# Optimization experiments

Hardware: AMD Instinct MI355X
Metric: run time of the kernel (lower is better)

The kernel has to match this reference:

```python
import jax, jax.numpy as jnp
import numpy as np

D_MODEL, D_STATE, D_CONV, EXPAND = 1024, 16, 4, 2
D_INNER = EXPAND * D_MODEL
BATCH, SEQ = 2, 2048


def setup_inputs() -> dict:
    key = jax.random.key(0)
    ks = jax.random.split(key, 10)
    inv = lambda n: 1.0 / np.sqrt(n)
    return {
        "x": jax.random.normal(ks[0], (BATCH, SEQ, D_MODEL), jnp.float32),
        "in_proj_w": jax.random.uniform(ks[1], (2 * D_INNER, D_MODEL), jnp.float32, -inv(D_MODEL), inv(D_MODEL)),
        "conv_w": jax.random.uniform(ks[2], (D_INNER, D_INNER, D_CONV), jnp.float32, -inv(D_INNER * D_CONV), inv(D_INNER * D_CONV)),
        "conv_b": jax.random.uniform(ks[3], (D_INNER,), jnp.float32, -inv(D_INNER * D_CONV), inv(D_INNER * D_CONV)),
        "dt_w": jax.random.uniform(ks[4], (D_INNER, D_INNER), jnp.float32, -inv(D_INNER), inv(D_INNER)),
        "dt_b": jax.random.uniform(ks[5], (D_INNER,), jnp.float32, -inv(D_INNER), inv(D_INNER)),
        "A_log": jax.random.normal(ks[6], (D_INNER, D_STATE), jnp.float32) * 0.01,
        "D": jnp.ones((D_INNER,), jnp.float32),
        "B_w": jax.random.uniform(ks[7], (D_STATE, D_INNER), jnp.float32, -inv(D_INNER), inv(D_INNER)),
        "C_w": jax.random.uniform(ks[8], (D_STATE, D_INNER), jnp.float32, -inv(D_INNER), inv(D_INNER)),
        "out_w": jax.random.uniform(ks[9], (D_MODEL, D_INNER), jnp.float32, -inv(D_INNER), inv(D_INNER)),
    }


def _forward(x, in_proj_w, conv_w, conv_b, dt_w, dt_b, A_log, D, B_w, C_w, out_w):
    xz = x @ in_proj_w.T                      # [b, l, 2*d_inner]
    xc, z = jnp.split(xz, 2, axis=-1)
    # causal depthful conv1d (full channel mixing, left-padded)
    h = jnp.transpose(xc, (0, 2, 1))          # [b, d, l]
    h = jnp.pad(h, ((0, 0), (0, 0), (D_CONV - 1, 0)))
    h = jax.lax.conv_general_dilated(h, conv_w, (1,), 'VALID',
                                     dimension_numbers=('NCH', 'OIH', 'NCH'))
    h = h + conv_b[None, :, None]
    u = jnp.transpose(h, (0, 2, 1))           # [b, l, d_inner]

    dt = jnp.clip(jax.nn.sigmoid(u @ dt_w.T + dt_b), 1e-4, 1.0)  # [b, l, d]
    A = -jnp.exp(A_log)                       # [d, n]
    Bm = u @ B_w.T                            # [b, l, n]
    Cm = u @ C_w.T                            # [b, l, n]

    # time-major scan over the recurrence
    u_t = jnp.transpose(u, (1, 0, 2))
    dt_t = jnp.transpose(dt, (1, 0, 2))
    B_t = jnp.transpose(Bm, (1, 0, 2))
    C_t = jnp.transpose(Cm, (1, 0, 2))

    def step(state, inp):
        ut, dtt, bt, ct = inp                 # [b,d], [b,d], [b,n], [b,n]
        dA = jnp.exp(jnp.clip(dtt[:, :, None] * A, -5.0, 5.0))   # [b,d,n]
        dB = dtt[:, :, None] * bt[:, None, :] * ut[:, :, None]   # [b,d,n]
        state = dA * state + dB + 1e-6
        y = jnp.sum(state * ct[:, None, :], axis=-1) + D * ut    # [b,d]
        return state, y

    state0 = jnp.zeros((x.shape[0], D_INNER, D_STATE), x.dtype)
    _, ys = jax.lax.scan(step, state0, (u_t, dt_t, B_t, C_t))
    y = jnp.transpose(ys, (1, 0, 2))          # [b, l, d_inner]
    y = y * jax.nn.silu(z)
    return y @ out_w.T                        # [b, l, d_model]


def reference(x, in_proj_w, conv_w, conv_b, dt_w, dt_b, A_log, D, B_w, C_w, out_w):
    return _forward(x, in_proj_w, conv_w, conv_b, dt_w, dt_b, A_log, D, B_w, C_w, out_w)
```

## Files before the change

### kernel.cpp

```cpp
#include <hip/hip_runtime.h>

#define BATCHN 2
#define SEQL   2048
#define DM     1024
#define DI     2048
#define DSN    16
#define MTOT   (BATCHN * SEQL)
#define PADL   (SEQL + 3)
#define NC     64
#define CL     (SEQL / NC)
#define BCKS   8

typedef __attribute__((ext_vector_type(8))) __bf16 bf16x8;
typedef __attribute__((ext_vector_type(4))) float f32x4;

__device__ __forceinline__ unsigned short f2b(float f) {
    union { float f; unsigned u; } v; v.f = f;
    unsigned r = v.u + 0x7FFF + ((v.u >> 16) & 1);
    return (unsigned short)(r >> 16);
}
__device__ __forceinline__ float b2f(unsigned short b) {
    union { float f; unsigned u; } v; v.u = ((unsigned)b) << 16;
    return v.f;
}

__device__ __forceinline__ void gl_lds16(const void* g, void* l) {
    __builtin_amdgcn_global_load_lds(
        (const __attribute__((address_space(1))) unsigned int*)g,
        (__attribute__((address_space(3))) unsigned int*)l, 16, 0, 0);
}

__device__ __forceinline__ void swz(int& bx, int& by) {
    int gx = gridDim.x, gy = gridDim.y;
    int lin = blockIdx.y * gx + blockIdx.x;
    int xcd = lin & 7, k = lin >> 3;
    int rw = gx >> 1, rh = gy >> 2;
    by = (xcd >> 1) * rh + k / rw;
    bx = (xcd & 1) * rw + k % rw;
}

#define NB_XCVT (MTOT * DM / 4 / 256)
__global__ void cvt_x_all(const float* __restrict__ src, unsigned short* __restrict__ dst) {
    int blk = blockIdx.x;
    if (blk < NB_XCVT) {
        int i = blk * 256 + threadIdx.x;
        int b = i >> 19;
        float4 v = ((const float4*)src)[i];
        ushort4 o;
        o.x = f2b(v.x); o.y = f2b(v.y); o.z = f2b(v.z); o.w = f2b(v.w);
        ((ushort4*)dst)[i + (b + 1) * (3 * DM / 4)] = o;
    } else {
        int i = (blk - NB_XCVT) * 256 + threadIdx.x;
        if (i < BATCHN * 3 * DM) {
            int b = i / (3 * DM);
            int r = i % (3 * DM);
            dst[(size_t)b * PADL * DM + r] = 0;
        }
    }
}

#define NB_CONVW (DI * DI / 256)
#define NB_TP    ((DM / 32) * (DI / 32))
#define NB_IPZ   (DI * DM / 4 / 256)
#define NB_DTW   (DI * DI / 4 / 256)
#define NB_OW    (DM * DI / 4 / 256)
#define NB_BW    (DSN * DI / 4 / 256 + 1)
__global__ void __launch_bounds__(256)
cvt_w_all(const float* __restrict__ convw, const float* __restrict__ ipw,
          const float* __restrict__ dtw, const float* __restrict__ ow,
          const float* __restrict__ bw, const float* __restrict__ cw,
          unsigned short* __restrict__ wk, unsigned short* __restrict__ Pt,
          unsigned short* __restrict__ ipz, unsigned short* __restrict__ dtwb,
          unsigned short* __restrict__ owb, unsigned short* __restrict__ bcb)
{
    __shared__ float tile[32][33];
    int blk = blockIdx.x;
    int t = threadIdx.x;
    if (blk < NB_CONVW) {
        int i = blk * 256 + t;
        float4 v = ((const float4*)convw)[i];
        wk[0 * (size_t)DI * DI + i] = f2b(v.x);
        wk[1 * (size_t)DI * DI + i] = f2b(v.y);
        wk[2 * (size_t)DI * DI + i] = f2b(v.z);
        wk[3 * (size_t)DI * DI + i] = f2b(v.w);
        return;
    }
    blk -= NB_CONVW;
    if (blk < NB_TP) {
        int ct = (blk & 31) * 32, it = (blk >> 5) * 32;
        int tx = t & 31, ty = t >> 5;
#pragma unroll
        for (int r = 0; r < 4; ++r)
            tile[ty + r * 8][tx] = ipw[(size_t)(it + ty + r * 8) * DM + ct + tx];
        __syncthreads();
#pragma unroll
        for (int r = 0; r < 4; ++r)
            Pt[(size_t)(ct + ty + r * 8) * DI + it + tx] = f2b(tile[tx][ty + r * 8]);
        return;
    }
    blk -= NB_TP;
    const float* src;
    unsigned short* dst;
    int n4;
    if (blk < NB_IPZ) {
        src = ipw + (size_t)DI * DM; dst = ipz; n4 = DI * DM / 4;
    } else if ((blk -= NB_IPZ) < NB_DTW) {
        src = dtw; dst = dtwb; n4 = DI * DI / 4;
    } else if ((blk -= NB_DTW) < NB_OW) {
        src = ow; dst = owb; n4 = DM * DI / 4;
    } else if ((blk -= NB_OW) < NB_BW) {
        src = bw; dst = bcb; n4 = DSN * DI / 4;
    } else {
        blk -= NB_BW;
        src = cw; dst = bcb + (size_t)DSN * DI; n4 = DSN * DI / 4;
    }
    int i = blk * 256 + t;
    if (i < n4) {
        float4 v = ((const float4*)src)[i];
        ushort4 o;
        o.x = f2b(v.x); o.y = f2b(v.y); o.z = f2b(v.z); o.w = f2b(v.w);
        ((ushort4*)dst)[i] = o;
    }
}

template<int MODE>
__global__ void __launch_bounds__(256)
gemm_bt(const unsigned short* __restrict__ Abase,
        const unsigned short* __restrict__ Bbase,
        const float* __restrict__ bias,
        unsigned short* __restrict__ out_bf,
        float* __restrict__ out_f,
        int K)
{
    __shared__ __align__(16) unsigned short As[128 * 64];
    __shared__ __align__(16) unsigned short Bs[128 * 64];

    const int t = threadIdx.x;
    const int lane = t & 63;
    const int wave = t >> 6;
    const int wm = wave & 1, wn = wave >> 1;
    int bx, by;
    swz(bx, by);
    const int m0 = by * 128, n0 = bx * 128;
    const int srow = t >> 3;
    const int scol = (t & 7) * 8;
    const int gcol = (((t & 7) ^ (srow & 7))) * 8;

    f32x4 acc[4][4];
#pragma unroll
    for (int i = 0; i < 4; ++i)
#pragma unroll
        for (int j = 0; j < 4; ++j)
            acc[i][j] = f32x4{0.f, 0.f, 0.f, 0.f};

    const unsigned short* arow[4];
    const unsigned short* brow[4];
#pragma unroll
    for (int i = 0; i < 4; ++i) {
        int rg = m0 + srow + i * 32;
        arow[i] = Abase + (size_t)rg * K;
        int ng = n0 + srow + i * 32;
        brow[i] = Bbase + (size_t)ng * K;
    }
    for (int k0 = 0; k0 < K; k0 += 64) {
#pragma unroll
        for (int i = 0; i < 4; ++i)
            gl_lds16(arow[i] + k0 + gcol, &As[(size_t)(srow + i * 32) * 64 + scol]);
#pragma unroll
        for (int i = 0; i < 4; ++i)
            gl_lds16(brow[i] + k0 + gcol, &Bs[(size_t)(srow + i * 32) * 64 + scol]);
        __syncthreads();
        const int qa = (lane >> 4) * 8;
        const int am = lane & 15;
        const int sw = (am & 7) << 3;
#pragma unroll
        for (int kk = 0; kk < 64; kk += 32) {
            bf16x8 af[4], bfv[4];
#pragma unroll
            for (int i = 0; i < 4; ++i)
                af[i] = *(const bf16x8*)&As[(wm * 64 + i * 16 + am) * 64 + ((kk + qa) ^ sw)];
#pragma unroll
            for (int j = 0; j < 4; ++j)
                bfv[j] = *(const bf16x8*)&Bs[(wn * 64 + j * 16 + am) * 64 + ((kk + qa) ^ sw)];
#pragma unroll
            for (int i = 0; i < 4; ++i)
#pragma unroll
                for (int j = 0; j < 4; ++j)
                    acc[i][j] = __builtin_amdgcn_mfma_f32_16x16x32_bf16(
                        af[i], bfv[j], acc[i][j], 0, 0, 0);
        }
        __syncthreads();
    }

    const int erow0 = m0 + wm * 64;
    const int ecol0 = n0 + wn * 64 + (lane & 15);
    const int rq = (lane >> 4) * 4;
#pragma unroll
    for (int i = 0; i < 4; ++i) {
#pragma unroll
        for (int j = 0; j < 4; ++j) {
            int col = ecol0 + j * 16;
#pragma unroll
            for (int r = 0; r < 4; ++r) {
                int row = erow0 + i * 16 + rq + r;
                float v = acc[i][j][r];
                if (MODE == 3) {
                    out_f[(size_t)row * DM + col] = v;
                } else {
                    out_bf[(size_t)row * DI + col] = f2b(v);
                }
            }
        }
    }
}


#define ABUF8(b) ((b) * 16384)
#define BBUF8(b) (32768 + (b) * 8192)

#define STA8(buf, Mh, kt) do { const int kc_ = ((kt) & NTM) << 6; \
    gl_lds16(pAst + (size_t)((Mh) * 32) * SA + kc_, &lds[ABUF8(buf) + (Mh) * 8192 + ldsw]); \
    gl_lds16(pAst + (size_t)((Mh) * 32 + 128) * SA + kc_, &lds[ABUF8(buf) + (Mh) * 8192 + 4096 + ldsw]); \
} while (0)
#define STB8(buf, Nh, kt) do { const int kc_ = ((kt) & NTM) << 6; \
    gl_lds16(pBst + (size_t)((Nh) * 32) * SB + kc_, &lds[BBUF8(buf) + (Nh) * 4096 + ldsw]); \
} while (0)

#define LA8(buf, Mh) \
    a00 = *(const bf16x8*)&lds[ABUF8(buf) + (Mh) * 8192 + ar + c0]; \
    a01 = *(const bf16x8*)&lds[ABUF8(buf) + (Mh) * 8192 + ar + c1]; \
    a10 = *(const bf16x8*)&lds[ABUF8(buf) + (Mh) * 8192 + ar + 1024 + c0]; \
    a11 = *(const bf16x8*)&lds[ABUF8(buf) + (Mh) * 8192 + ar + 1024 + c1];
#define LB8(buf, Nh) \
    b00 = *(const bf16x8*)&lds[BBUF8(buf) + (Nh) * 4096 + br + c0]; \
    b01 = *(const bf16x8*)&lds[BBUF8(buf) + (Nh) * 4096 + br + c1]; \
    b10 = *(const bf16x8*)&lds[BBUF8(buf) + (Nh) * 4096 + br + 1024 + c0]; \
    b11 = *(const bf16x8*)&lds[BBUF8(buf) + (Nh) * 4096 + br + 1024 + c1];

#define MM8(Mh, Nh) \
    acc[(Mh)*2][(Nh)*2]     = __builtin_amdgcn_mfma_f32_16x16x32_bf16(a00, b00, acc[(Mh)*2][(Nh)*2], 0, 0, 0); \
    acc[(Mh)*2][(Nh)*2+1]   = __builtin_amdgcn_mfma_f32_16x16x32_bf16(a00, b10, acc[(Mh)*2][(Nh)*2+1], 0, 0, 0); \
    acc[(Mh)*2+1][(Nh)*2]   = __builtin_amdgcn_mfma_f32_16x16x32_bf16(a10, b00, acc[(Mh)*2+1][(Nh)*2], 0, 0, 0); \
    acc[(Mh)*2+1][(Nh)*2+1] = __builtin_amdgcn_mfma_f32_16x16x32_bf16(a10, b10, acc[(Mh)*2+1][(Nh)*2+1], 0, 0, 0); \
    acc[(Mh)*2][(Nh)*2]     = __builtin_amdgcn_mfma_f32_16x16x32_bf16(a01, b01, acc[(Mh)*2][(Nh)*2], 0, 0, 0); \
    acc[(Mh)*2][(Nh)*2+1]   = __builtin_amdgcn_mfma_f32_16x16x32_bf16(a01, b11, acc[(Mh)*2][(Nh)*2+1], 0, 0, 0); \
    acc[(Mh)*2+1][(Nh)*2]   = __builtin_amdgcn_mfma_f32_16x16x32_bf16(a11, b01, acc[(Mh)*2+1][(Nh)*2], 0, 0, 0); \
    acc[(Mh)*2+1][(Nh)*2+1] = __builtin_amdgcn_mfma_f32_16x16x32_bf16(a11, b11, acc[(Mh)*2+1][(Nh)*2+1], 0, 0, 0);

#define PH_MID \
    __builtin_amdgcn_s_barrier(); \
    asm volatile("s_waitcnt lgkmcnt(0)" ::: "memory"); \
    __builtin_amdgcn_sched_barrier(0); \
    __builtin_amdgcn_s_setprio(1);
#define PH_END \
    __builtin_amdgcn_s_setprio(0); \
    __builtin_amdgcn_s_barrier(); \
    __builtin_amdgcn_sched_barrier(0);
#define PH_END_W \
    __builtin_amdgcn_s_setprio(0); \
    asm volatile("s_waitcnt vmcnt(3)" ::: "memory"); \
    __builtin_amdgcn_s_barrier(); \
    __builtin_amdgcn_sched_barrier(0);

template<int MODE>
__global__ void __launch_bounds__(512, 1)
gemm8(const unsigned short* __restrict__ Abase,
      const unsigned short* __restrict__ Bbase,
      const float* __restrict__ bias,
      unsigned short* __restrict__ out_bf,
      float* __restrict__ out_f)
{
    constexpr int K   = (MODE == 0) ? 1024 : (MODE == 1) ? 4096 : 2048;
    constexpr int SA  = (MODE == 2 || MODE == 4) ? 2048 : 1024;
    constexpr int SB  = (MODE == 0) ? 1024 : (MODE == 1) ? 4096 : 2048;
    constexpr int NT  = K / 64;
    constexpr int NTM = NT - 1;
    constexpr int NI  = NT / 2;
    (void)out_f;

    __shared__ __align__(16) unsigned short lds[49152];

    const int t = threadIdx.x;
    const int lane = t & 63;
    const int wave = t >> 6;
    const int wm = wave >> 1;
    const int wn = wave & 1;
    int bx, by;
    swz(bx, by);
    const int m0 = by * 256, n0 = bx * 128;

    const unsigned short* Ap;
    if (MODE == 0)      Ap = Abase + ((size_t)(m0 >> 11) * PADL + 3 + (m0 & 2047)) * DM;
    else if (MODE == 1) Ap = Abase + ((size_t)(m0 >> 11) * PADL + (m0 & 2047)) * DM;
    else if (MODE == 4) Ap = Abase + (size_t)blockIdx.z * DI * DI + (size_t)m0 * SA;
    else                Ap = Abase + (size_t)m0 * SA;
    const unsigned short* Bp = Bbase + (size_t)n0 * SB;

    const int tr = t >> 3;
    const int rowg = ((tr >> 5) << 6) + (tr & 31);
    const int gcolb = ((t & 7) ^ (tr & 7)) << 3;
    const unsigned short* pAst = Ap + (size_t)rowg * SA + gcolb;
    const unsigned short* pBst = Bp + (size_t)rowg * SB + gcolb;
    const int ldsw = t * 8;

    const int am = lane & 15;
    const int qa = (lane >> 4) << 3;
    const int sw = (am & 7) << 3;
    const int c0 = qa ^ sw;
    const int c1 = (32 + qa) ^ sw;
    const int ar = wm * 2048 + am * 64;
    const int br = wn * 2048 + am * 64;

    f32x4 acc[4][4];
#pragma unroll
    for (int i = 0; i < 4; ++i)
#pragma unroll
        for (int j = 0; j < 4; ++j)
            acc[i][j] = f32x4{0.f, 0.f, 0.f, 0.f};

    bf16x8 a00, a01, a10, a11, b00, b01, b10, b11;

    STA8(0, 0, 0); STB8(0, 1, 0); STA8(0, 1, 0); STB8(0, 0, 0);
    STA8(1, 0, 1); STB8(1, 1, 1);
    asm volatile("s_waitcnt vmcnt(3)" ::: "memory");
    __builtin_amdgcn_s_barrier();
    __builtin_amdgcn_sched_barrier(0);

#pragma unroll 1
    for (int it = 0; it < NI; ++it) {
        const int ko  = 2 * it + 1;
        const int ke  = (2 * it + 2) & NTM;
        const int ko2 = (2 * it + 3) & NTM;
        LA8(0, 0) LB8(0, 0) STA8(1, 1, ko);
        PH_MID MM8(0, 0) PH_END
        LB8(0, 1) STB8(1, 0, ko);
        PH_MID MM8(0, 1) PH_END
        LA8(0, 1) STA8(0, 0, ke);
        PH_MID MM8(1, 1) PH_END
        LB8(0, 0) STB8(0, 1, ke);
        PH_MID MM8(1, 0) PH_END_W
        LA8(1, 0) LB8(1, 0) STA8(0, 1, ke);
        PH_MID MM8(0, 0) PH_END
        LB8(1, 1) STB8(0, 0, ke);
        PH_MID MM8(0, 1) PH_END
        LA8(1, 1) STA8(1, 0, ko2);
        PH_MID MM8(1, 1) PH_END
        LB8(1, 0) STB8(1, 1, ko2);
        PH_MID MM8(1, 0) PH_END_W
    }

    asm volatile("s_waitcnt vmcnt(0)" ::: "memory");

    const int rq = (lane >> 4) << 2;
    const int er = m0 + wm * 64;
    const int ec = n0 + wn * 64 + am;
#pragma unroll
    for (int mi = 0; mi < 4; ++mi) {
#pragma unroll
        for (int nj = 0; nj < 4; ++nj) {
            int col = ec + nj * 16;
#pragma unroll
            for (int r = 0; r < 4; ++r) {
                int row = er + mi * 16 + rq + r;
                float v = acc[mi][nj][r];
                if (MODE == 0) {
                    out_bf[(size_t)row * DI + col] = f2b(v);
                } else if (MODE == 1) {
                    v += bias[col];
                    out_bf[(size_t)row * DI + col] = f2b(v);
                } else if (MODE == 2) {
                    v += bias[col];
                    float s = 1.f / (1.f + __expf(-v));
                    s = fminf(fmaxf(s, 1e-4f), 1.f);
                    out_bf[(size_t)row * DI + col] = f2b(s);
                } else {
                    out_bf[(size_t)row * 4096 + (size_t)blockIdx.z * 1024 + col] = f2b(v);
                }
            }
        }
    }
}

__global__ void __launch_bounds__(256)
bc_mfma(const unsigned short* __restrict__ u,
        const unsigned short* __restrict__ w,
        float* __restrict__ pc)
{
    const int t = threadIdx.x;
    const int lane = t & 63;
    const int wave = t >> 6;
    const int ks = blockIdx.x;
    const int m0 = blockIdx.y * 128 + wave * 32;
    const int am = lane & 15, quad = lane >> 4;

    f32x4 acc[2][2];
#pragma unroll
    for (int i = 0; i < 2; ++i)
#pragma unroll
        for (int j = 0; j < 2; ++j)
            acc[i][j] = f32x4{0.f, 0.f, 0.f, 0.f};

    const int kbase = ks * (DI / BCKS);
    const unsigned short* ur0 = u + (size_t)(m0 + am) * DI;
    const unsigned short* ur1 = u + (size_t)(m0 + 16 + am) * DI;
    const unsigned short* wr0 = w + (size_t)am * DI;
    const unsigned short* wr1 = w + (size_t)(16 + am) * DI;
#pragma unroll 2
    for (int kk = 0; kk < DI / BCKS; kk += 32) {
        int k = kbase + kk + quad * 8;
        bf16x8 a0 = *(const bf16x8*)(ur0 + k);
        bf16x8 a1 = *(const bf16x8*)(ur1 + k);
        bf16x8 b0 = *(const bf16x8*)(wr0 + k);
        bf16x8 b1 = *(const bf16x8*)(wr1 + k);
        acc[0][0] = __builtin_amdgcn_mfma_f32_16x16x32_bf16(a0, b0, acc[0][0], 0, 0, 0);
        acc[0][1] = __builtin_amdgcn_mfma_f32_16x16x32_bf16(a0, b1, acc[0][1], 0, 0, 0);
        acc[1][0] = __builtin_amdgcn_mfma_f32_16x16x32_bf16(a1, b0, acc[1][0], 0, 0, 0);
        acc[1][1] = __builtin_amdgcn_mfma_f32_16x16x32_bf16(a1, b1, acc[1][1], 0, 0, 0);
    }
    float* base = pc + (size_t)ks * MTOT * 32;
#pragma unroll
    for (int i = 0; i < 2; ++i)
#pragma unroll
        for (int j = 0; j < 2; ++j)
#pragma unroll
            for (int r = 0; r < 4; ++r) {
                int row = m0 + i * 16 + quad * 4 + r;
                int col = j * 16 + am;
                base[(size_t)row * 32 + col] = acc[i][j][r];
            }
}

__global__ void __launch_bounds__(256)
bc_reduce(const float* __restrict__ pc, float* __restrict__ outf)
{
    int i = blockIdx.x * 256 + threadIdx.x;
    const float4* p4 = (const float4*)pc;
    float4 s = p4[i];
#pragma unroll
    for (int ks = 1; ks < BCKS; ++ks) {
        float4 v = p4[(size_t)ks * (MTOT * 8) + i];
        s.x += v.x; s.y += v.y; s.z += v.z; s.w += v.w;
    }
    ((float4*)outf)[i] = s;
}

__global__ void __launch_bounds__(256)
scan_p1(const unsigned short* __restrict__ dt_bf,
        const unsigned short* __restrict__ u_bf,
        const float* __restrict__ bcf,
        const float* __restrict__ A_log,
        float* __restrict__ Pbuf,
        float* __restrict__ Sbuf)
{
    const int t = threadIdx.x;
    const int blk = blockIdx.x;
    const int c  = blk & (NC - 1);
    const int dh = (blk >> 6) & 7;
    const int b  = blk >> 9;
    const int d  = dh * 256 + t;

    float Adn[16];
    {
        const float4* ar = (const float4*)(A_log + (size_t)d * DSN);
#pragma unroll
        for (int q = 0; q < 4; ++q) {
            float4 v = ar[q];
            Adn[q * 4 + 0] = -__expf(v.x);
            Adn[q * 4 + 1] = -__expf(v.y);
            Adn[q * 4 + 2] = -__expf(v.z);
            Adn[q * 4 + 3] = -__expf(v.w);
        }
    }
    float s[16], P[16];
#pragma unroll
    for (int n = 0; n < 16; ++n) { s[n] = 0.f; P[n] = 1.f; }

    const size_t rowbase = (size_t)b * SEQL + (size_t)c * CL;
    for (int l0 = 0; l0 < CL; l0 += 4) {
        float dt4[4], u4[4];
#pragma unroll
        for (int j = 0; j < 4; ++j) {
            size_t rb = rowbase + l0 + j;
            dt4[j] = b2f(dt_bf[rb * DI + d]);
            u4[j] = b2f(u_bf[rb * DI + d]);
        }
#pragma unroll
        for (int j = 0; j < 4; ++j) {
            size_t rb = rowbase + l0 + j;
            const float4* Br = (const float4*)(bcf + rb * 32);
            float Bn[16];
#pragma unroll
            for (int q = 0; q < 4; ++q) {
                float4 v = Br[q];
                Bn[q * 4 + 0] = v.x; Bn[q * 4 + 1] = v.y;
                Bn[q * 4 + 2] = v.z; Bn[q * 4 + 3] = v.w;
            }
            float dt = dt4[j];
            float dBu = dt * u4[j];
#pragma unroll
            for (int n = 0; n < 16; ++n) {
                float x = dt * Adn[n];
                x = fminf(fmaxf(x, -5.f), 5.f);
                float dA = __expf(x);
                P[n] *= dA;
                s[n] = dA * s[n] + (dBu * Bn[n] + 1e-6f);
            }
        }
    }
    size_t ob = (((size_t)c * BATCHN + b) * DI + d) * DSN;
#pragma unroll
    for (int q = 0; q < 4; ++q) {
        ((float4*)(Pbuf + ob))[q] = make_float4(P[q*4], P[q*4+1], P[q*4+2], P[q*4+3]);
        ((float4*)(Sbuf + ob))[q] = make_float4(s[q*4], s[q*4+1], s[q*4+2], s[q*4+3]);
    }
}

__global__ void __launch_bounds__(256)
scan_p2(const float* __restrict__ Pbuf,
        const float* __restrict__ Sbuf,
        float* __restrict__ Ibuf)
{
    const int i = blockIdx.x * 256 + threadIdx.x;
    const int stride = BATCHN * DI * DSN;
    float s = 0.f;
    for (int c0 = 0; c0 < NC; c0 += 8) {
        float Pv[8], Sv[8];
#pragma unroll
        for (int j = 0; j < 8; ++j) {
            size_t idx = (size_t)(c0 + j) * stride + i;
            Pv[j] = Pbuf[idx];
            Sv[j] = Sbuf[idx];
        }
#pragma unroll
        for (int j = 0; j < 8; ++j) {
            size_t idx = (size_t)(c0 + j) * stride + i;
            Ibuf[idx] = s;
            s = Pv[j] * s + Sv[j];
        }
    }
}

__global__ void __launch_bounds__(256)
scan_p3(const unsigned short* __restrict__ dt_bf,
        const unsigned short* __restrict__ u_bf,
        const float* __restrict__ bcf,
        const unsigned short* __restrict__ z_bf,
        const float* __restrict__ A_log,
        const float* __restrict__ Dvec,
        const float* __restrict__ Ibuf,
        unsigned short* __restrict__ y_bf)
{
    const int t = threadIdx.x;
    const int blk = blockIdx.x;
    const int c  = blk & (NC - 1);
    const int dh = (blk >> 6) & 7;
    const int b  = blk >> 9;
    const int d  = dh * 256 + t;

    float Adn[16];
    {
        const float4* ar = (const float4*)(A_log + (size_t)d * DSN);
#pragma unroll
        for (int q = 0; q < 4; ++q) {
            float4 v = ar[q];
            Adn[q * 4 + 0] = -__expf(v.x);
            Adn[q * 4 + 1] = -__expf(v.y);
            Adn[q * 4 + 2] = -__expf(v.z);
            Adn[q * 4 + 3] = -__expf(v.w);
        }
    }
    const float Dd = Dvec[d];
    float s[16];
    {
        size_t ib = (((size_t)c * BATCHN + b) * DI + d) * DSN;
#pragma unroll
        for (int q = 0; q < 4; ++q) {
            float4 v = ((const float4*)(Ibuf + ib))[q];
            s[q * 4 + 0] = v.x; s[q * 4 + 1] = v.y;
            s[q * 4 + 2] = v.z; s[q * 4 + 3] = v.w;
        }
    }

    const size_t rowbase = (size_t)b * SEQL + (size_t)c * CL;
    for (int l0 = 0; l0 < CL; l0 += 4) {
        float dt4[4], u4[4], z4[4];
#pragma unroll
        for (int j = 0; j < 4; ++j) {
            size_t rb = rowbase + l0 + j;
            dt4[j] = b2f(dt_bf[rb * DI + d]);
            u4[j] = b2f(u_bf[rb * DI + d]);
            z4[j] = b2f(z_bf[rb * DI + d]);
        }
#pragma unroll
        for (int j = 0; j < 4; ++j) {
            size_t rb = rowbase + l0 + j;
            const float4* Br = (const float4*)(bcf + rb * 32);
            float Bn[16], Cn[16];
#pragma unroll
            for (int q = 0; q < 4; ++q) {
                float4 v = Br[q];
                Bn[q * 4 + 0] = v.x; Bn[q * 4 + 1] = v.y;
                Bn[q * 4 + 2] = v.z; Bn[q * 4 + 3] = v.w;
                float4 w = Br[q + 4];
                Cn[q * 4 + 0] = w.x; Cn[q * 4 + 1] = w.y;
                Cn[q * 4 + 2] = w.z; Cn[q * 4 + 3] = w.w;
            }
            float dt = dt4[j];
            float dBu = dt * u4[j];
            float y = 0.f;
#pragma unroll
            for (int n = 0; n < 16; ++n) {
                float x = dt * Adn[n];
                x = fminf(fmaxf(x, -5.f), 5.f);
                float dA = __expf(x);
                s[n] = dA * s[n] + (dBu * Bn[n] + 1e-6f);
                y += s[n] * Cn[n];
            }
            y += Dd * u4[j];
            float zz = z4[j];
            y *= zz / (1.f + __expf(-zz));
            y_bf[rb * DI + d] = f2b(y);
        }
    }
}

extern "C" void kernel_launch(void* const* d_in, const int* in_sizes, int n_in,
                              void* d_out, int out_size, void* d_ws, size_t ws_size,
                              hipStream_t stream) {
    const float* x     = (const float*)d_in[0];
    const float* ipw   = (const float*)d_in[1];
    const float* convw = (const float*)d_in[2];
    const float* convb = (const float*)d_in[3];
    const float* dtw   = (const float*)d_in[4];
    const float* dtb   = (const float*)d_in[5];
    const float* alog  = (const float*)d_in[6];
    const float* dvec  = (const float*)d_in[7];
    const float* bw    = (const float*)d_in[8];
    const float* cwm   = (const float*)d_in[9];
    const float* ow    = (const float*)d_in[10];
    float* out = (float*)d_out;

    char* ws = (char*)d_ws;
    size_t off = 0;
    auto carve = [&](size_t bytes) {
        char* p = ws + off;
        off += (bytes + 255) & ~(size_t)255;
        return p;
    };
    unsigned short* xpad   = (unsigned short*)carve((size_t)BATCHN * PADL * DM * 2);
    unsigned short* ipz_bf = (unsigned short*)carve((size_t)DI * DM * 2);
    unsigned short* Pt_bf  = (unsigned short*)carve((size_t)DM * DI * 2);
    unsigned short* wk_bf  = (unsigned short*)carve((size_t)4 * DI * DI * 2);
    unsigned short* mk_bf  = (unsigned short*)carve((size_t)4 * DI * DM * 2);
    unsigned short* dtw_bf = (unsigned short*)carve((size_t)DI * DI * 2);
    unsigned short* ow_bf  = (unsigned short*)carve((size_t)DM * DI * 2);
    unsigned short* bc_bf  = (unsigned short*)carve((size_t)2 * DSN * DI * 2);
    unsigned short* z_bf   = (unsigned short*)carve((size_t)MTOT * DI * 2);
    unsigned short* u_bf   = (unsigned short*)carve((size_t)MTOT * DI * 2);
    unsigned short* dt_bf  = (unsigned short*)carve((size_t)MTOT * DI * 2);
    float*          bc_f   = (float*)carve((size_t)MTOT * 2 * DSN * 4);
    unsigned short* y_bf   = (unsigned short*)carve((size_t)MTOT * DI * 2);
    float*          Pbuf   = (float*)carve((size_t)NC * BATCHN * DI * DSN * 4);
    float*          Sbuf   = (float*)carve((size_t)NC * BATCHN * DI * DSN * 4);
    float*          Ibuf   = (float*)carve((size_t)NC * BATCHN * DI * DSN * 4);
    float*          pc_f   = (float*)carve((size_t)BCKS * MTOT * 32 * 4);

    cvt_x_all<<<NB_XCVT + (BATCHN * 3 * DM + 255) / 256, 256, 0, stream>>>(x, xpad);
    {
        int nb = NB_CONVW + NB_TP + NB_IPZ + NB_DTW + NB_OW + 2 * NB_BW;
        cvt_w_all<<<nb, 256, 0, stream>>>(convw, ipw, dtw, ow, bw, cwm,
                                          wk_bf, Pt_bf, ipz_bf, dtw_bf, ow_bf, bc_bf);
    }

    gemm8<4><<<dim3(8, 8, 4), 512, 0, stream>>>(wk_bf, Pt_bf, nullptr, mk_bf, nullptr);
    gemm8<0><<<dim3(16, 16), 512, 0, stream>>>(xpad, ipz_bf, nullptr, z_bf, nullptr);
    gemm8<1><<<dim3(16, 16), 512, 0, stream>>>(xpad, mk_bf, convb, u_bf, nullptr);
    bc_mfma<<<dim3(BCKS, MTOT / 128), 256, 0, stream>>>(u_bf, bc_bf, pc_f);
    bc_reduce<<<MTOT * 32 / 4 / 256, 256, 0, stream>>>(pc_f, bc_f);
    gemm8<2><<<dim3(16, 16), 512, 0, stream>>>(u_bf, dtw_bf, dtb, dt_bf, nullptr);
    scan_p1<<<BATCHN * 8 * NC, 256, 0, stream>>>(dt_bf, u_bf, bc_f, alog, Pbuf, Sbuf);
    scan_p2<<<BATCHN * DI * DSN / 256, 256, 0, stream>>>(Pbuf, Sbuf, Ibuf);
    scan_p3<<<BATCHN * 8 * NC, 256, 0, stream>>>(dt_bf, u_bf, bc_f, z_bf, alog, dvec, Ibuf, y_bf);
    gemm_bt<3><<<dim3(8, 32), 256, 0, stream>>>(y_bf, ow_bf, nullptr, nullptr, out, DI);
}
```

Baseline: 466.3 us.

## Replace 8-phase GEMM schedule with full-tile register double-buffered pipeline

```diff
diff --git a/kernel.cpp b/kernel.cpp
--- a/kernel.cpp
+++ b/kernel.cpp
@@ -215,52 +215,40 @@
 }
 
 
-#define ABUF8(b) ((b) * 16384)
-#define BBUF8(b) (32768 + (b) * 8192)
-
-#define STA8(buf, Mh, kt) do { const int kc_ = ((kt) & NTM) << 6; \
-    gl_lds16(pAst + (size_t)((Mh) * 32) * SA + kc_, &lds[ABUF8(buf) + (Mh) * 8192 + ldsw]); \
-    gl_lds16(pAst + (size_t)((Mh) * 32 + 128) * SA + kc_, &lds[ABUF8(buf) + (Mh) * 8192 + 4096 + ldsw]); \
+#define STAGE(buf, kt) do { \
+    const int kc_ = ((kt) & NTM) << 6; \
+    gl_lds16(pA + 0 * 64 * SA + kc_, &lds[(buf) * 16384 + ldsA + 0 * 4096]); \
+    gl_lds16(pA + 1 * 64 * SA + kc_, &lds[(buf) * 16384 + ldsA + 1 * 4096]); \
+    gl_lds16(pA + 2 * 64 * SA + kc_, &lds[(buf) * 16384 + ldsA + 2 * 4096]); \
+    gl_lds16(pA + 3 * 64 * SA + kc_, &lds[(buf) * 16384 + ldsA + 3 * 4096]); \
+    gl_lds16(pB + 0 * 64 * SB + kc_, &lds[32768 + (buf) * 8192 + ldsB + 0 * 4096]); \
+    gl_lds16(pB + 1 * 64 * SB + kc_, &lds[32768 + (buf) * 8192 + ldsB + 1 * 4096]); \
 } while (0)
-#define STB8(buf, Nh, kt) do { const int kc_ = ((kt) & NTM) << 6; \
-    gl_lds16(pBst + (size_t)((Nh) * 32) * SB + kc_, &lds[BBUF8(buf) + (Nh) * 4096 + ldsw]); \
+
+#define LOADF(AF, BF, buf) do { \
+    const unsigned short* _ab = &lds[(buf) * 16384 + arow]; \
+    const unsigned short* _bb = &lds[32768 + (buf) * 8192 + brow]; \
+    _Pragma("unroll") \
+    for (int _i = 0; _i < 4; ++_i) { \
+        AF[_i][0] = *(const bf16x8*)&_ab[_i * 1024 + c0]; \
+        AF[_i][1] = *(const bf16x8*)&_ab[_i * 1024 + c1]; \
+    } \
+    _Pragma("unroll") \
+    for (int _j = 0; _j < 4; ++_j) { \
+        BF[_j][0] = *(const bf16x8*)&_bb[_j * 1024 + c0]; \
+        BF[_j][1] = *(const bf16x8*)&_bb[_j * 1024 + c1]; \
+    } \
 } while (0)
 
-#define LA8(buf, Mh) \
-    a00 = *(const bf16x8*)&lds[ABUF8(buf) + (Mh) * 8192 + ar + c0]; \
-    a01 = *(const bf16x8*)&lds[ABUF8(buf) + (Mh) * 8192 + ar + c1]; \
-    a10 = *(const bf16x8*)&lds[ABUF8(buf) + (Mh) * 8192 + ar + 1024 + c0]; \
-    a11 = *(const bf16x8*)&lds[ABUF8(buf) + (Mh) * 8192 + ar + 1024 + c1];
-#define LB8(buf, Nh) \
-    b00 = *(const bf16x8*)&lds[BBUF8(buf) + (Nh) * 4096 + br + c0]; \
-    b01 = *(const bf16x8*)&lds[BBUF8(buf) + (Nh) * 4096 + br + c1]; \
-    b10 = *(const bf16x8*)&lds[BBUF8(buf) + (Nh) * 4096 + br + 1024 + c0]; \
-    b11 = *(const bf16x8*)&lds[BBUF8(buf) + (Nh) * 4096 + br + 1024 + c1];
-
-#define MM8(Mh, Nh) \
-    acc[(Mh)*2][(Nh)*2]     = __builtin_amdgcn_mfma_f32_16x16x32_bf16(a00, b00, acc[(Mh)*2][(Nh)*2], 0, 0, 0); \
-    acc[(Mh)*2][(Nh)*2+1]   = __builtin_amdgcn_mfma_f32_16x16x32_bf16(a00, b10, acc[(Mh)*2][(Nh)*2+1], 0, 0, 0); \
-    acc[(Mh)*2+1][(Nh)*2]   = __builtin_amdgcn_mfma_f32_16x16x32_bf16(a10, b00, acc[(Mh)*2+1][(Nh)*2], 0, 0, 0); \
-    acc[(Mh)*2+1][(Nh)*2+1] = __builtin_amdgcn_mfma_f32_16x16x32_bf16(a10, b10, acc[(Mh)*2+1][(Nh)*2+1], 0, 0, 0); \
-    acc[(Mh)*2][(Nh)*2]     = __builtin_amdgcn_mfma_f32_16x16x32_bf16(a01, b01, acc[(Mh)*2][(Nh)*2], 0, 0, 0); \
-    acc[(Mh)*2][(Nh)*2+1]   = __builtin_amdgcn_mfma_f32_16x16x32_bf16(a01, b11, acc[(Mh)*2][(Nh)*2+1], 0, 0, 0); \
-    acc[(Mh)*2+1][(Nh)*2]   = __builtin_amdgcn_mfma_f32_16x16x32_bf16(a11, b01, acc[(Mh)*2+1][(Nh)*2], 0, 0, 0); \
-    acc[(Mh)*2+1][(Nh)*2+1] = __builtin_amdgcn_mfma_f32_16x16x32_bf16(a11, b11, acc[(Mh)*2+1][(Nh)*2+1], 0, 0, 0);
-
-#define PH_MID \
-    __builtin_amdgcn_s_barrier(); \
-    asm volatile("s_waitcnt lgkmcnt(0)" ::: "memory"); \
-    __builtin_amdgcn_sched_barrier(0); \
-    __builtin_amdgcn_s_setprio(1);
-#define PH_END \
-    __builtin_amdgcn_s_setprio(0); \
-    __builtin_amdgcn_s_barrier(); \
-    __builtin_amdgcn_sched_barrier(0);
-#define PH_END_W \
-    __builtin_amdgcn_s_setprio(0); \
-    asm volatile("s_waitcnt vmcnt(3)" ::: "memory"); \
-    __builtin_amdgcn_s_barrier(); \
-    __builtin_amdgcn_sched_barrier(0);
+#define MME(AF, BF) do { \
+    _Pragma("unroll") \
+    for (int _i = 0; _i < 4; ++_i) \
+    _Pragma("unroll") \
+    for (int _j = 0; _j < 4; ++_j) { \
+        acc[_i][_j] = __builtin_amdgcn_mfma_f32_16x16x32_bf16(AF[_i][0], BF[_j][0], acc[_i][_j], 0, 0, 0); \
+        acc[_i][_j] = __builtin_amdgcn_mfma_f32_16x16x32_bf16(AF[_i][1], BF[_j][1], acc[_i][_j], 0, 0, 0); \
+    } \
+} while (0)
 
 template<int MODE>
 __global__ void __launch_bounds__(512, 1)
@@ -296,20 +284,20 @@
     else                Ap = Abase + (size_t)m0 * SA;
     const unsigned short* Bp = Bbase + (size_t)n0 * SB;
 
-    const int tr = t >> 3;
-    const int rowg = ((tr >> 5) << 6) + (tr & 31);
-    const int gcolb = ((t & 7) ^ (tr & 7)) << 3;
-    const unsigned short* pAst = Ap + (size_t)rowg * SA + gcolb;
-    const unsigned short* pBst = Bp + (size_t)rowg * SB + gcolb;
-    const int ldsw = t * 8;
+    const int strow = t >> 3;
+    const int gcs = ((t & 7) ^ (strow & 7)) * 8;
+    const unsigned short* pA = Ap + (size_t)strow * SA + gcs;
+    const unsigned short* pB = Bp + (size_t)strow * SB + gcs;
+    const int ldsA = t * 8;
+    const int ldsB = t * 8;
 
     const int am = lane & 15;
     const int qa = (lane >> 4) << 3;
     const int sw = (am & 7) << 3;
     const int c0 = qa ^ sw;
     const int c1 = (32 + qa) ^ sw;
-    const int ar = wm * 2048 + am * 64;
-    const int br = wn * 2048 + am * 64;
+    const int arow = (wm * 64 + am) * 64;
+    const int brow = (wn * 64 + am) * 64;
 
     f32x4 acc[4][4];
 #pragma unroll
@@ -318,38 +306,42 @@
         for (int j = 0; j < 4; ++j)
             acc[i][j] = f32x4{0.f, 0.f, 0.f, 0.f};
 
-    bf16x8 a00, a01, a10, a11, b00, b01, b10, b11;
-
-    STA8(0, 0, 0); STB8(0, 1, 0); STA8(0, 1, 0); STB8(0, 0, 0);
-    STA8(1, 0, 1); STB8(1, 1, 1);
-    asm volatile("s_waitcnt vmcnt(3)" ::: "memory");
+    bf16x8 aX[4][2], bX[4][2], aY[4][2], bY[4][2];
+
+    STAGE(0, 0);
+    STAGE(1, 1);
+    asm volatile("s_waitcnt vmcnt(6)" ::: "memory");
     __builtin_amdgcn_s_barrier();
     __builtin_amdgcn_sched_barrier(0);
+    LOADF(aX, bX, 0);
 
 #pragma unroll 1
     for (int it = 0; it < NI; ++it) {
-        const int ko  = 2 * it + 1;
-        const int ke  = (2 * it + 2) & NTM;
-        const int ko2 = (2 * it + 3) & NTM;
-        LA8(0, 0) LB8(0, 0) STA8(1, 1, ko);
-        PH_MID MM8(0, 0) PH_END
-        LB8(0, 1) STB8(1, 0, ko);
-        PH_MID MM8(0, 1) PH_END
-        LA8(0, 1) STA8(0, 0, ke);
-        PH_MID MM8(1, 1) PH_END
-        LB8(0, 0) STB8(0, 1, ke);
-        PH_MID MM8(1, 0) PH_END_W
-        LA8(1, 0) LB8(1, 0) STA8(0, 1, ke);
-        PH_MID MM8(0, 0) PH_END
-        LB8(1, 1) STB8(0, 0, ke);
-        PH_MID MM8(0, 1) PH_END
-        LA8(1, 1) STA8(1, 0, ko2);
-        PH_MID MM8(1, 1) PH_END
-        LB8(1, 0) STB8(1, 1, ko2);
-        PH_MID MM8(1, 0) PH_END_W
-    }
-
-    asm volatile("s_waitcnt vmcnt(0)" ::: "memory");
+        asm volatile("s_waitcnt lgkmcnt(0)" ::: "memory");
+        __builtin_amdgcn_s_barrier();
+        __builtin_amdgcn_sched_barrier(0);
+        STAGE(0, 2 * it + 2);
+        asm volatile("s_waitcnt vmcnt(6)" ::: "memory");
+        __builtin_amdgcn_s_barrier();
+        __builtin_amdgcn_sched_barrier(0);
+        LOADF(aY, bY, 1);
+        __builtin_amdgcn_s_setprio(1);
+        MME(aX, bX);
+        __builtin_amdgcn_s_setprio(0);
+        asm volatile("s_waitcnt lgkmcnt(0)" ::: "memory");
+        __builtin_amdgcn_s_barrier();
+        __builtin_amdgcn_sched_barrier(0);
+        STAGE(1, 2 * it + 3);
+        asm volatile("s_waitcnt vmcnt(6)" ::: "memory");
+        __builtin_amdgcn_s_barrier();
+        __builtin_amdgcn_sched_barrier(0);
+        LOADF(aX, bX, 0);
+        __builtin_amdgcn_s_setprio(1);
+        MME(aY, bY);
+        __builtin_amdgcn_s_setprio(0);
+    }
+
+    asm volatile("s_waitcnt vmcnt(0) lgkmcnt(0)" ::: "memory");
 
     const int rq = (lane >> 4) << 2;
     const int er = m0 + wm * 64;
```

Result: no change. 466.3 us (-0.0%).
